# Kernel optimization log

Hardware: AMD Instinct MI355X
Metric: run time of the kernel (lower is better)

The kernel has to match this reference:

```python
import jax, jax.numpy as jnp
import numpy as np

D = 256   # hidden_dim
N = 1024  # total nodes
NP = 384  # paratope nodes
NE = 384  # epitope nodes
NC = 14   # atom channels


def setup_inputs() -> dict:
    key = jax.random.key(0)
    ks = jax.random.split(key, 24)
    s = 1.0 / np.sqrt(D)
    s3 = 1.0 / np.sqrt(3 * D)
    w = lambda k, shape, sc: (jax.random.normal(k, shape, jnp.float32) * sc)
    z = lambda: jnp.zeros((D,), jnp.float32)
    return {
        "H": w(ks[0], (N, D), 1.0),
        "X": w(ks[1], (N, NC, 3), 1.0),
        "paratope_mask": jnp.zeros((N,), bool).at[:NP].set(True),
        "epitope_mask": jnp.zeros((N,), bool).at[NP:NP + NE].set(True),
        "res_w1": w(ks[2], (1, D), 1.0), "res_b1": z(),
        "res_w2": w(ks[3], (D, D), s), "res_b2": z(),
        "atom_w1": w(ks[4], (1, D), 1.0), "atom_b1": z(),
        "atom_w2": w(ks[5], (D, D), s), "atom_b2": z(),
        "sim_weight": jnp.float32(0.5),
        "int_w1": w(ks[6], (3 * D, D), s3), "int_b1": z(),
        "int_w2": w(ks[7], (D, D), s), "int_b2": z(),
        "wl": w(ks[8], (D, D), s),
        "wr": w(ks[9], (D, D), s),
        "wg_w": w(ks[10], (D, D), s), "wg_b": z(),
        "wq_w": w(ks[11], (D, D), s), "wq_b": z(),
        "wk_w": w(ks[12], (D, D), s), "wk_b": z(),
        "wv_w": w(ks[13], (D, D), s), "wv_b": z(),
    }


def _mlp2(x, w1, b1, w2, b2):
    return jax.nn.silu(x @ w1 + b1) @ w2 + b2


def reference(H, X, paratope_mask, epitope_mask,
              res_w1, res_b1, res_w2, res_b2,
              atom_w1, atom_b1, atom_w2, atom_b2,
              sim_weight,
              int_w1, int_b1, int_w2, int_b2,
              wl, wr, wg_w, wg_b, wq_w, wq_b, wk_w, wk_b, wv_w, wv_b):
    p_idx = jnp.nonzero(paratope_mask, size=NP)[0]
    e_idx = jnp.nonzero(epitope_mask, size=NE)[0]
    Hp = H[p_idx]                      # [NP, D]
    He = H[e_idx]                      # [NE, D]
    Xp_ca = X[p_idx, 1]                # [NP, 3] (CA atom)
    Xe_ca = X[e_idx, 1]                # [NE, 3]

    dX = Xp_ca[:, None, :] - Xe_ca[None, :, :]         # [NP, NE, 3]
    S = jnp.sum(dX * dX, axis=-1, keepdims=True)       # [NP, NE, 1]
    # original computes S_residue and S_atom with identical formula
    S_res = _mlp2(S, res_w1, res_b1, res_w2, res_b2)
    S_atom = _mlp2(S, atom_w1, atom_b1, atom_w2, atom_b2)
    wmix = jax.nn.sigmoid(sim_weight)
    S_comb = wmix * S_res + (1.0 - wmix) * S_atom      # [NP, NE, D]

    Hp_e = jnp.broadcast_to(Hp[:, None, :], (NP, NE, D))
    He_e = jnp.broadcast_to(He[None, :, :], (NP, NE, D))
    Z_in = jnp.concatenate([Hp_e, He_e, S_comb], axis=-1)  # [NP, NE, 3D]
    Z = _mlp2(Z_in, int_w1, int_b1, int_w2, int_b2)        # [NP, NE, D]

    I = (Hp @ wl)[:, None, :] * (He @ wr)[None, :, :]      # outer-product interaction
    gate = jax.nn.sigmoid(Z @ wg_w + wg_b)
    f_tri = gate * I

    Q = Z @ wq_w + wq_b
    K = Z @ wk_w + wk_b
    V = Z @ wv_w + wv_b
    scores = jnp.einsum('ped,pfd->pef', Q, K) / (D ** 0.5)  # [NP, NE, NE]
    A = jax.nn.softmax(scores, axis=-1)
    f_att = jnp.einsum('pef,pfd->ped', A, V)

    H_tri = f_tri + f_att                                   # [NP, NE, D]
    return H.at[p_idx].set(H_tri.mean(axis=1))
```

## Files before the change

### kernel.cpp

```cpp
#include <hip/hip_runtime.h>

#define NPAR 384
#define NEPI 384
#define DD   256
#define NTAB 4096
#define SMAX 96.0f
#define SDELTA (SMAX / NTAB)
#define SINVD (NTAB / SMAX)

using bf16x8 = __bf16 __attribute__((ext_vector_type(8)));
using bf16x2 = __bf16 __attribute__((ext_vector_type(2)));
using f32x4  = float __attribute__((ext_vector_type(4)));

#if defined(__has_builtin)
#if __has_builtin(__builtin_amdgcn_cvt_pk_bf16_f32)
#define HAVE_PK_BF16 1
#endif
#endif

__device__ __forceinline__ float sigm(float x) { return 1.0f / (1.0f + __expf(-x)); }
__device__ __forceinline__ float silu(float x) { return x / (1.0f + __expf(-x)); }
__device__ __forceinline__ unsigned short f2bf(float f) {
  unsigned u = __float_as_uint(f);
  u += 0x7fffu + ((u >> 16) & 1u);
  return (unsigned short)(u >> 16);
}
__device__ __forceinline__ float bf2f(unsigned u16) {
  return __uint_as_float(u16 << 16);
}
__device__ __forceinline__ float bf2f_lo(unsigned w) {
  return __uint_as_float(w << 16);
}
__device__ __forceinline__ float bf2f_hi(unsigned w) {
  return __uint_as_float(w & 0xffff0000u);
}
__device__ __forceinline__ uint2 pack4(float a, float b, float c, float d) {
  uint2 r;
#ifdef HAVE_PK_BF16
  bf16x2 lo = __builtin_amdgcn_cvt_pk_bf16_f32(a, b);
  bf16x2 hi = __builtin_amdgcn_cvt_pk_bf16_f32(c, d);
  r.x = __builtin_bit_cast(unsigned, lo);
  r.y = __builtin_bit_cast(unsigned, hi);
#else
  r.x = (unsigned)f2bf(a) | ((unsigned)f2bf(b) << 16);
  r.y = (unsigned)f2bf(c) | ((unsigned)f2bf(d) << 16);
#endif
  return r;
}


__global__ void prep_kernel(
    const float* __restrict__ H, const float* __restrict__ wl,
    const float* __restrict__ wr, const float* __restrict__ int_w1,
    const float* __restrict__ res_w2, const float* __restrict__ atom_w2,
    const float* __restrict__ res_b2, const float* __restrict__ atom_b2,
    const float* __restrict__ int_b1, const float* __restrict__ simw,
    const float* __restrict__ wq_b, const float* __restrict__ wk_w,
    float* __restrict__ Hpl, float* __restrict__ Her,
    float* __restrict__ P1, float* __restrict__ P2,
    float* __restrict__ MrF, float* __restrict__ MaF,
    float* __restrict__ cvec, float* __restrict__ gv,
    float* __restrict__ wkT) {
  __shared__ float tile[32][33];
  const int b = blockIdx.x, t = threadIdx.x;
  if (b < 64) {
    const int bx = b & 7, by = b >> 3;
    const int tx = t & 31, ty = t >> 5;
    for (int r = 0; r < 32; r += 8)
      tile[ty + r][tx] = wk_w[(by * 32 + ty + r) * 256 + bx * 32 + tx];
    __syncthreads();
    for (int r = 0; r < 32; r += 8)
      wkT[(bx * 32 + ty + r) * 256 + by * 32 + tx] = tile[tx][ty + r];
  } else if (b < 576) {
    const int bb = b - 64;
    const int i = bb & 255;
    const bool isMa = bb >= 256;
    const float wmix = 1.0f / (1.0f + __expf(-simw[0]));
    const float sc = isMa ? (1.0f - wmix) : wmix;
    const float* W2 = isMa ? atom_w2 : res_w2;
    float acc = 0.f;
#pragma unroll 8
    for (int k = 0; k < 256; ++k)
      acc += W2[i * 256 + k] * int_w1[(512 + k) * 256 + t];
    (isMa ? MaF : MrF)[i * 256 + t] = acc * sc;
  } else if (b < 584) {
    const int bb = b - 576;
    const float wmix = 1.0f / (1.0f + __expf(-simw[0]));
    float acc = (bb == 0) ? int_b1[t] : 0.f;
#pragma unroll
    for (int k = bb * 32; k < bb * 32 + 32; ++k) {
      float bm = wmix * res_b2[k] + (1.0f - wmix) * atom_b2[k];
      acc += bm * int_w1[(512 + k) * 256 + t];
    }
    atomicAdd(&cvec[t], acc);
  } else if (b < 648) {
    const int lane = t & 63, w = t >> 6;
    const int d = (b - 584) * 4 + w;
    float acc = 0.f;
#pragma unroll
    for (int i = 0; i < 4; ++i) {
      const int c = i * 64 + lane;
      acc += wk_w[d * 256 + c] * wq_b[c];
    }
    acc += __shfl_xor(acc, 1);
    acc += __shfl_xor(acc, 2);
    acc += __shfl_xor(acc, 4);
    acc += __shfl_xor(acc, 8);
    acc += __shfl_xor(acc, 16);
    acc += __shfl_xor(acc, 32);
    if (lane == 0) gv[d] = acc;
  } else {
    const int idx = b - 648;
    const int seg = idx / 384, r = idx % 384;
    const float* A;
    const float* B;
    float* C;
    switch (seg) {
      case 0:  A = H + r * 256;            B = wl;              C = Hpl + r * 256; break;
      case 1:  A = H + (NPAR + r) * 256;   B = wr;              C = Her + r * 256; break;
      case 2:  A = H + r * 256;            B = int_w1;          C = P1 + r * 256;  break;
      default: A = H + (NPAR + r) * 256;   B = int_w1 + 65536;  C = P2 + r * 256;  break;
    }
    float acc = 0.f;
#pragma unroll 8
    for (int k = 0; k < 256; ++k)
      acc += A[k] * B[k * 256 + t];
    C[t] = acc;
  }
}

__global__ void mm_rows(const float* __restrict__ A, const float* __restrict__ B,
                        float* __restrict__ C) {
  const int r = blockIdx.x, j = threadIdx.x;
  float acc = 0.f;
#pragma unroll 8
  for (int k = 0; k < 256; ++k)
    acc += A[r * 256 + k] * B[k * 256 + j];
  C[r * 256 + j] = acc;
}

__global__ void pack_kernel(const float* __restrict__ MrF, const float* __restrict__ MaF,
                            const float* __restrict__ w2, const float* __restrict__ wg,
                            const float* __restrict__ WqkF, unsigned short* __restrict__ wpack) {
  const int idx = blockIdx.x * 256 + threadIdx.x;
  const int m = idx >> 16;
  const int r = idx & 65535;
  const int chunk = r >> 9;
  const int lane = (r >> 3) & 63;
  const int j = r & 7;
  const int k = (chunk >> 4) * 32 + (lane >> 4) * 8 + j;
  const int n = (chunk & 15) * 16 + (lane & 15);
  const float* src;
  switch (m) {
    case 0: src = MrF; break;
    case 1: src = MaF; break;
    case 2: src = w2; break;
    case 3: src = wg; break;
    default: src = WqkF; break;
  }
  wpack[idx] = f2bf(src[k * 256 + n]);
}


__device__ __forceinline__ void zero_acc4(f32x4 (&acc)[4][4]) {
#pragma unroll
  for (int mt = 0; mt < 4; ++mt)
#pragma unroll
    for (int nt = 0; nt < 4; ++nt)
      acc[mt][nt] = (f32x4){0.f, 0.f, 0.f, 0.f};
}

__device__ __forceinline__ void gemm4(f32x4 (&acc)[4][4],
                                      const unsigned short* __restrict__ wp,
                                      const unsigned short* ub, int lane, int wv) {
  const int l15 = lane & 15, l4 = lane >> 4;
#pragma unroll
  for (int ks = 0; ks < 8; ++ks) {
    bf16x8 a[4];
#pragma unroll
    for (int mt = 0; mt < 4; ++mt)
      a[mt] = *reinterpret_cast<const bf16x8*>(wp + ((ks * 16 + wv * 4 + mt) * 64 + lane) * 8);
#pragma unroll
    for (int nt = 0; nt < 4; ++nt) {
      bf16x8 b = *reinterpret_cast<const bf16x8*>(ub + (nt * 16 + l15) * 264 + ks * 32 + l4 * 8);
#pragma unroll
      for (int mt = 0; mt < 4; ++mt)
        acc[mt][nt] = __builtin_amdgcn_mfma_f32_16x16x32_bf16(a[mt], b, acc[mt][nt], 0, 0, 0);
    }
  }
}

__device__ __forceinline__ void fill_u(unsigned short* ub, const float* Sv,
                                       const float* __restrict__ w1,
                                       const float* __restrict__ b1, int t) {
  const int dg = t & 31, rb = t >> 5;
  const f32x4 w1a = *reinterpret_cast<const f32x4*>(&w1[dg * 8]);
  const f32x4 w1b = *reinterpret_cast<const f32x4*>(&w1[dg * 8 + 4]);
  const f32x4 b1a = *reinterpret_cast<const f32x4*>(&b1[dg * 8]);
  const f32x4 b1b = *reinterpret_cast<const f32x4*>(&b1[dg * 8 + 4]);
#pragma unroll
  for (int i = 0; i < 8; ++i) {
    const int e = rb + i * 8;
    const float s = Sv[e];
    uint2 lo = pack4(silu(fmaf(s, w1a[0], b1a[0])), silu(fmaf(s, w1a[1], b1a[1])),
                     silu(fmaf(s, w1a[2], b1a[2])), silu(fmaf(s, w1a[3], b1a[3])));
    uint2 hi = pack4(silu(fmaf(s, w1b[0], b1b[0])), silu(fmaf(s, w1b[1], b1b[1])),
                     silu(fmaf(s, w1b[2], b1b[2])), silu(fmaf(s, w1b[3], b1b[3])));
    uint4 pk = {lo.x, lo.y, hi.x, hi.y};
    *reinterpret_cast<uint4*>(&ub[e * 264 + dg * 8]) = pk;
  }
}


__global__ __launch_bounds__(256, 3) void tab_kernel(
    const float* __restrict__ res_w1, const float* __restrict__ res_b1,
    const float* __restrict__ atom_w1, const float* __restrict__ atom_b1,
    const unsigned short* __restrict__ wpack, unsigned short* __restrict__ tab) {
  __shared__ __align__(16) unsigned short ubuf[64 * 264];
  __shared__ float Sv[64];
  const int t = threadIdx.x, lane = t & 63, wv = t >> 6;
  const int l15 = lane & 15, l4 = lane >> 4;
  const int n0 = blockIdx.x * 64;
  if (t < 64) Sv[t] = (n0 + t) * SDELTA;
  __syncthreads();
  f32x4 acc[4][4];
  zero_acc4(acc);
  fill_u(ubuf, Sv, res_w1, res_b1, t);
  __syncthreads();
  gemm4(acc, wpack + 0 * 65536, ubuf, lane, wv);
  __syncthreads();
  fill_u(ubuf, Sv, atom_w1, atom_b1, t);
  __syncthreads();
  gemm4(acc, wpack + 1 * 65536, ubuf, lane, wv);
#pragma unroll
  for (int mt = 0; mt < 4; ++mt) {
    const int d = wv * 64 + mt * 16 + l4 * 4;
#pragma unroll
    for (int nt = 0; nt < 4; ++nt) {
      const int n = n0 + nt * 16 + l15;
      *reinterpret_cast<uint2*>(&tab[n * 256 + d]) =
          pack4(acc[mt][nt][0], acc[mt][nt][1], acc[mt][nt][2], acc[mt][nt][3]);
    }
  }
}


__global__ __launch_bounds__(256, 3) void pair_kernel(
    const float* __restrict__ Xg, const unsigned short* __restrict__ tab,
    const float* __restrict__ int_b2, const float* __restrict__ wg_b,
    const unsigned short* __restrict__ wpack, const float* __restrict__ cvec,
    const float* __restrict__ P1, const float* __restrict__ P2,
    const float* __restrict__ Hpl, const float* __restrict__ Her,
    float* __restrict__ ftri, unsigned short* __restrict__ Zsw) {
  __shared__ __align__(16) unsigned short ubuf[64 * 264];
  __shared__ float Sv[64];
  __shared__ float pc[DD];
  const int t = threadIdx.x, lane = t & 63, wv = t >> 6;
  const int l15 = lane & 15, l4 = lane >> 4;
  const int p = blockIdx.x / 6, cc = blockIdx.x % 6, e0 = cc * 64;
  const int d0 = wv * 64;

  if (t < 64) {
    const int e = e0 + t;
    float dx = Xg[p * 42 + 3] - Xg[(NPAR + e) * 42 + 3];
    float dy = Xg[p * 42 + 4] - Xg[(NPAR + e) * 42 + 4];
    float dz = Xg[p * 42 + 5] - Xg[(NPAR + e) * 42 + 5];
    Sv[t] = dx * dx + dy * dy + dz * dz;
  }
  pc[t] = P1[p * DD + t] + cvec[t];
  __syncthreads();

  {
    const int dg = t & 31, rb = t >> 5;
    const f32x4 pca = *reinterpret_cast<const f32x4*>(&pc[dg * 8]);
    const f32x4 pcb = *reinterpret_cast<const f32x4*>(&pc[dg * 8 + 4]);
#pragma unroll
    for (int i = 0; i < 8; ++i) {
      const int e = rb + i * 8;
      float sv = Sv[e] * SINVD;
      int idx = (int)sv;
      idx = idx > (NTAB - 2) ? (NTAB - 2) : idx;
      const float fr = sv - (float)idx;
      const uint4 t0 = *reinterpret_cast<const uint4*>(&tab[idx * 256 + dg * 8]);
      const uint4 t1 = *reinterpret_cast<const uint4*>(&tab[(idx + 1) * 256 + dg * 8]);
      const f32x4 p2a = *reinterpret_cast<const f32x4*>(&P2[(e0 + e) * DD + dg * 8]);
      const f32x4 p2b = *reinterpret_cast<const f32x4*>(&P2[(e0 + e) * DD + dg * 8 + 4]);
      float z0 = bf2f_lo(t0.x), z1 = bf2f_hi(t0.x), z2 = bf2f_lo(t0.y), z3 = bf2f_hi(t0.y);
      float z4 = bf2f_lo(t0.z), z5 = bf2f_hi(t0.z), z6 = bf2f_lo(t0.w), z7 = bf2f_hi(t0.w);
      z0 = fmaf(fr, bf2f_lo(t1.x) - z0, z0) + pca[0] + p2a[0];
      z1 = fmaf(fr, bf2f_hi(t1.x) - z1, z1) + pca[1] + p2a[1];
      z2 = fmaf(fr, bf2f_lo(t1.y) - z2, z2) + pca[2] + p2a[2];
      z3 = fmaf(fr, bf2f_hi(t1.y) - z3, z3) + pca[3] + p2a[3];
      z4 = fmaf(fr, bf2f_lo(t1.z) - z4, z4) + pcb[0] + p2b[0];
      z5 = fmaf(fr, bf2f_hi(t1.z) - z5, z5) + pcb[1] + p2b[1];
      z6 = fmaf(fr, bf2f_lo(t1.w) - z6, z6) + pcb[2] + p2b[2];
      z7 = fmaf(fr, bf2f_hi(t1.w) - z7, z7) + pcb[3] + p2b[3];
      uint2 lo = pack4(silu(z0), silu(z1), silu(z2), silu(z3));
      uint2 hi = pack4(silu(z4), silu(z5), silu(z6), silu(z7));
      uint4 pk = {lo.x, lo.y, hi.x, hi.y};
      *reinterpret_cast<uint4*>(&ubuf[e * 264 + dg * 8]) = pk;
    }
  }
  __syncthreads();

  f32x4 acc[4][4];
  zero_acc4(acc);
  gemm4(acc, wpack + 2 * 65536, ubuf, lane, wv);
  __syncthreads();
#pragma unroll
  for (int mt = 0; mt < 4; ++mt) {
    const int d = d0 + mt * 16 + l4 * 4;
    const f32x4 bb = *reinterpret_cast<const f32x4*>(&int_b2[d]);
#pragma unroll
    for (int nt = 0; nt < 4; ++nt) {
      const int e = nt * 16 + l15;
      *reinterpret_cast<uint2*>(&ubuf[e * 264 + d]) =
          pack4(acc[mt][nt][0] + bb[0], acc[mt][nt][1] + bb[1],
                acc[mt][nt][2] + bb[2], acc[mt][nt][3] + bb[3]);
    }
  }
  __syncthreads();

  {
    unsigned short* Zd = Zsw + (size_t)p * 98304 + (size_t)(cc * 4 + wv) * 4096 + lane * 8;
#pragma unroll
    for (int ks = 0; ks < 8; ++ks) {
      *reinterpret_cast<uint4*>(Zd + ks * 512) =
          *reinterpret_cast<const uint4*>(&ubuf[(wv * 16 + l15) * 264 + ks * 32 + l4 * 8]);
    }
  }

  zero_acc4(acc);
  gemm4(acc, wpack + 3 * 65536, ubuf, lane, wv);
#pragma unroll
  for (int mt = 0; mt < 4; ++mt) {
    const int d = d0 + mt * 16 + l4 * 4;
    const f32x4 bb = *reinterpret_cast<const f32x4*>(&wg_b[d]);
    const f32x4 hl = *reinterpret_cast<const f32x4*>(&Hpl[p * DD + d]);
    f32x4 fs = (f32x4){0.f, 0.f, 0.f, 0.f};
#pragma unroll
    for (int nt = 0; nt < 4; ++nt) {
      const int e = e0 + nt * 16 + l15;
      const f32x4 hr = *reinterpret_cast<const f32x4*>(&Her[e * DD + d]);
#pragma unroll
      for (int r = 0; r < 4; ++r)
        fs[r] += sigm(acc[mt][nt][r] + bb[r]) * hr[r];
    }
#pragma unroll
    for (int r = 0; r < 4; ++r) {
      float v = fs[r] * hl[r];
      v += __shfl_xor(v, 1);
      v += __shfl_xor(v, 2);
      v += __shfl_xor(v, 4);
      v += __shfl_xor(v, 8);
      if (l15 == 0) atomicAdd(&ftri[p * DD + d + r], v);
    }
  }
}


__global__ __launch_bounds__(256, 3) void attn_kernel(
    const unsigned short* __restrict__ Zsw, const float* __restrict__ gv,
    const unsigned short* __restrict__ wpack, float* __restrict__ cbufg) {
  __shared__ __align__(16) unsigned short Tc[64 * 264];
  __shared__ float red[256];
  __shared__ float red2[256];
  const int t = threadIdx.x, lane = t & 63, wv = t >> 6;
  const int l15 = lane & 15, l4 = lane >> 4;
  const int xcd = blockIdx.x & 7, inner = blockIdx.x >> 3;
  const int p = (inner / 6) * 8 + xcd, c = inner % 6;
  const unsigned short* Zsp = Zsw + (size_t)p * 98304;
  const unsigned short* wqk = wpack + 4 * 65536;

  {
    f32x4 ta[4][4];
#pragma unroll
    for (int mt = 0; mt < 4; ++mt)
#pragma unroll
      for (int nt = 0; nt < 4; ++nt) ta[mt][nt] = (f32x4){0.f, 0.f, 0.f, 0.f};
    const unsigned short* Tb = Zsp + (size_t)(c * 4) * 4096 + lane * 8;
    bf16x8 bcur[4], bnxt[4];
#pragma unroll
    for (int nt = 0; nt < 4; ++nt)
      bcur[nt] = *reinterpret_cast<const bf16x8*>(Tb + nt * 4096);
#pragma unroll
    for (int ks = 0; ks < 8; ++ks) {
      if (ks < 7) {
#pragma unroll
        for (int nt = 0; nt < 4; ++nt)
          bnxt[nt] = *reinterpret_cast<const bf16x8*>(Tb + nt * 4096 + (ks + 1) * 512);
      }
      bf16x8 a[4];
#pragma unroll
      for (int mt = 0; mt < 4; ++mt)
        a[mt] = *reinterpret_cast<const bf16x8*>(wqk + ((ks * 16 + wv * 4 + mt) * 64 + lane) * 8);
#pragma unroll
      for (int nt = 0; nt < 4; ++nt)
#pragma unroll
        for (int mt = 0; mt < 4; ++mt)
          ta[mt][nt] = __builtin_amdgcn_mfma_f32_16x16x32_bf16(a[mt], bcur[nt], ta[mt][nt], 0, 0, 0);
      if (ks < 7) {
#pragma unroll
        for (int nt = 0; nt < 4; ++nt) bcur[nt] = bnxt[nt];
      }
    }
#pragma unroll
    for (int mt = 0; mt < 4; ++mt) {
      const int d = wv * 64 + mt * 16 + l4 * 4;
      const f32x4 gq = *reinterpret_cast<const f32x4*>(&gv[d]);
#pragma unroll
      for (int nt = 0; nt < 4; ++nt) {
        const int e = nt * 16 + l15;
        *reinterpret_cast<uint2*>(&Tc[e * 264 + d]) =
            pack4((ta[mt][nt][0] + gq[0]) * 0.0625f, (ta[mt][nt][1] + gq[1]) * 0.0625f,
                  (ta[mt][nt][2] + gq[2]) * 0.0625f, (ta[mt][nt][3] + gq[3]) * 0.0625f);
      }
    }
  }
  __syncthreads();

  f32x4 sc[4][6];
#pragma unroll
  for (int mt = 0; mt < 4; ++mt)
#pragma unroll
    for (int s = 0; s < 6; ++s) sc[mt][s] = (f32x4){0.f, 0.f, 0.f, 0.f};

  {
    const unsigned short* Sb = Zsp + (size_t)wv * 4096 + lane * 8;
    bf16x8 b0[3], b1[3];
#pragma unroll
    for (int j = 0; j < 3; ++j)
      b0[j] = *reinterpret_cast<const bf16x8*>(Sb + j * 16384);
#pragma unroll
    for (int ks = 0; ks < 8; ++ks) {
#pragma unroll
      for (int j = 0; j < 3; ++j)
        b1[j] = *reinterpret_cast<const bf16x8*>(Sb + (3 + j) * 16384 + ks * 512);
      bf16x8 a[4];
#pragma unroll
      for (int mt = 0; mt < 4; ++mt)
        a[mt] = *reinterpret_cast<const bf16x8*>(&Tc[(mt * 16 + l15) * 264 + ks * 32 + l4 * 8]);
#pragma unroll
      for (int j = 0; j < 3; ++j)
#pragma unroll
        for (int mt = 0; mt < 4; ++mt)
          sc[mt][j] = __builtin_amdgcn_mfma_f32_16x16x32_bf16(a[mt], b0[j], sc[mt][j], 0, 0, 0);
      if (ks < 7) {
#pragma unroll
        for (int j = 0; j < 3; ++j)
          b0[j] = *reinterpret_cast<const bf16x8*>(Sb + j * 16384 + (ks + 1) * 512);
      }
#pragma unroll
      for (int j = 0; j < 3; ++j)
#pragma unroll
        for (int mt = 0; mt < 4; ++mt)
          sc[mt][3 + j] = __builtin_amdgcn_mfma_f32_16x16x32_bf16(a[mt], b1[j], sc[mt][3 + j], 0, 0, 0);
    }
  }

  float rmax[4][4];
#pragma unroll
  for (int mt = 0; mt < 4; ++mt) {
#pragma unroll
    for (int r = 0; r < 4; ++r) {
      float m = -1e30f;
#pragma unroll
      for (int s = 0; s < 6; ++s) m = fmaxf(m, sc[mt][s][r]);
      m = fmaxf(m, __shfl_xor(m, 1));
      m = fmaxf(m, __shfl_xor(m, 2));
      m = fmaxf(m, __shfl_xor(m, 4));
      m = fmaxf(m, __shfl_xor(m, 8));
      rmax[mt][r] = m;
    }
  }
  if (l15 == 0) {
#pragma unroll
    for (int mt = 0; mt < 4; ++mt)
#pragma unroll
      for (int r = 0; r < 4; ++r)
        red[wv * 64 + mt * 16 + l4 * 4 + r] = rmax[mt][r];
  }
  __syncthreads();
#pragma unroll
  for (int mt = 0; mt < 4; ++mt) {
#pragma unroll
    for (int r = 0; r < 4; ++r) {
      const int row = mt * 16 + l4 * 4 + r;
      rmax[mt][r] = fmaxf(fmaxf(red[row], red[64 + row]), fmaxf(red[128 + row], red[192 + row]));
    }
  }

  float rsum[4][4];
#pragma unroll
  for (int mt = 0; mt < 4; ++mt) {
#pragma unroll
    for (int r = 0; r < 4; ++r) {
      float sSum = 0.f;
#pragma unroll
      for (int s = 0; s < 6; ++s) {
        float e = __expf(sc[mt][s][r] - rmax[mt][r]);
        sc[mt][s][r] = e;
        sSum += e;
      }
      sSum += __shfl_xor(sSum, 1);
      sSum += __shfl_xor(sSum, 2);
      sSum += __shfl_xor(sSum, 4);
      sSum += __shfl_xor(sSum, 8);
      rsum[mt][r] = sSum;
    }
  }
  if (l15 == 0) {
#pragma unroll
    for (int mt = 0; mt < 4; ++mt)
#pragma unroll
      for (int r = 0; r < 4; ++r)
        red2[wv * 64 + mt * 16 + l4 * 4 + r] = rsum[mt][r];
  }
  __syncthreads();
  float rinv[4][4];
#pragma unroll
  for (int mt = 0; mt < 4; ++mt) {
#pragma unroll
    for (int r = 0; r < 4; ++r) {
      const int row = mt * 16 + l4 * 4 + r;
      rinv[mt][r] = 1.0f / (red2[row] + red2[64 + row] + red2[128 + row] + red2[192 + row]);
    }
  }

#pragma unroll
  for (int s = 0; s < 6; ++s) {
    float v = 0.f;
#pragma unroll
    for (int mt = 0; mt < 4; ++mt)
#pragma unroll
      for (int r = 0; r < 4; ++r)
        v += sc[mt][s][r] * rinv[mt][r];
    v += __shfl_xor(v, 16);
    v += __shfl_xor(v, 32);
    if (lane < 16)
      atomicAdd(&cbufg[p * NEPI + s * 64 + wv * 16 + lane], v);
  }
}


__global__ __launch_bounds__(256) void out_kernel(
    const unsigned short* __restrict__ Zsw, const float* __restrict__ ftri,
    const float* __restrict__ cbufg, const float* __restrict__ wvw,
    const float* __restrict__ wvb, float* __restrict__ out) {
  __shared__ float cb[NEPI];
  __shared__ float part[16][257];
  __shared__ float u[DD];
  const int p = blockIdx.x, t = threadIdx.x;
  const int lane = t & 63, wv = t >> 6;
  const int l15 = lane & 15, l4 = lane >> 4;
  for (int i = t; i < NEPI; i += 256) cb[i] = cbufg[p * NEPI + i];
  __syncthreads();
  const unsigned short* Zsp = Zsw + (size_t)p * 98304;
  float a16[16];
#pragma unroll
  for (int j = 0; j < 16; ++j) a16[j] = 0.f;
#pragma unroll 4
  for (int grp = 0; grp < 24; ++grp) {
    const float w = cb[grp * 16 + l15];
    const uint4 z0 = *reinterpret_cast<const uint4*>(Zsp + grp * 4096 + wv * 512 + lane * 8);
    const uint4 z1 = *reinterpret_cast<const uint4*>(Zsp + grp * 4096 + (wv + 4) * 512 + lane * 8);
    a16[0] = fmaf(w, bf2f(z0.x & 0xffffu), a16[0]);
    a16[1] = fmaf(w, bf2f(z0.x >> 16), a16[1]);
    a16[2] = fmaf(w, bf2f(z0.y & 0xffffu), a16[2]);
    a16[3] = fmaf(w, bf2f(z0.y >> 16), a16[3]);
    a16[4] = fmaf(w, bf2f(z0.z & 0xffffu), a16[4]);
    a16[5] = fmaf(w, bf2f(z0.z >> 16), a16[5]);
    a16[6] = fmaf(w, bf2f(z0.w & 0xffffu), a16[6]);
    a16[7] = fmaf(w, bf2f(z0.w >> 16), a16[7]);
    a16[8]  = fmaf(w, bf2f(z1.x & 0xffffu), a16[8]);
    a16[9]  = fmaf(w, bf2f(z1.x >> 16), a16[9]);
    a16[10] = fmaf(w, bf2f(z1.y & 0xffffu), a16[10]);
    a16[11] = fmaf(w, bf2f(z1.y >> 16), a16[11]);
    a16[12] = fmaf(w, bf2f(z1.z & 0xffffu), a16[12]);
    a16[13] = fmaf(w, bf2f(z1.z >> 16), a16[13]);
    a16[14] = fmaf(w, bf2f(z1.w & 0xffffu), a16[14]);
    a16[15] = fmaf(w, bf2f(z1.w >> 16), a16[15]);
  }
#pragma unroll
  for (int j = 0; j < 8; ++j) part[l15][wv * 32 + l4 * 8 + j] = a16[j];
#pragma unroll
  for (int j = 0; j < 8; ++j) part[l15][128 + wv * 32 + l4 * 8 + j] = a16[8 + j];
  __syncthreads();
  float uu = 0.f;
#pragma unroll
  for (int g = 0; g < 16; ++g) uu += part[g][t];
  u[t] = uu;
  __syncthreads();
  float acc = ftri[p * DD + t] + 384.0f * wvb[t];
#pragma unroll 8
  for (int d = 0; d < DD; ++d)
    acc = fmaf(u[d], wvw[d * DD + t], acc);
  out[p * DD + t] = acc * (1.0f / 384.0f);
}


extern "C" void kernel_launch(void* const* d_in, const int* in_sizes, int n_in,
                              void* d_out, int out_size, void* d_ws, size_t ws_size,
                              hipStream_t stream) {
  (void)in_sizes; (void)n_in; (void)out_size; (void)ws_size;
  const float* H = (const float*)d_in[0];
  const float* X = (const float*)d_in[1];
  const float* res_w1 = (const float*)d_in[4];
  const float* res_b1 = (const float*)d_in[5];
  const float* res_w2 = (const float*)d_in[6];
  const float* res_b2 = (const float*)d_in[7];
  const float* atom_w1 = (const float*)d_in[8];
  const float* atom_b1 = (const float*)d_in[9];
  const float* atom_w2 = (const float*)d_in[10];
  const float* atom_b2 = (const float*)d_in[11];
  const float* simw = (const float*)d_in[12];
  const float* int_w1 = (const float*)d_in[13];
  const float* int_b1 = (const float*)d_in[14];
  const float* int_w2 = (const float*)d_in[15];
  const float* int_b2 = (const float*)d_in[16];
  const float* wl = (const float*)d_in[17];
  const float* wr = (const float*)d_in[18];
  const float* wg_w = (const float*)d_in[19];
  const float* wg_b = (const float*)d_in[20];
  const float* wq_w = (const float*)d_in[21];
  const float* wq_b = (const float*)d_in[22];
  const float* wk_w = (const float*)d_in[23];
  const float* wv_w = (const float*)d_in[25];
  const float* wv_b = (const float*)d_in[26];

  char* ws = (char*)d_ws;
  unsigned short* wpack = (unsigned short*)(ws + 0);
  float* MrF   = (float*)(ws + 655360);
  float* MaF   = (float*)(ws + 917504);
  float* WqkF  = (float*)(ws + 1179648);
  float* wkT   = (float*)(ws + 1441792);
  float* cvec  = (float*)(ws + 1703936);
  float* gv    = (float*)(ws + 1704960);
  float* P1    = (float*)(ws + 1705984);
  float* P2    = (float*)(ws + 2099200);
  float* Hpl   = (float*)(ws + 2492416);
  float* Her   = (float*)(ws + 2885632);
  float* ftri  = (float*)(ws + 3278848);
  float* cbufg = (float*)(ws + 3672064);
  unsigned short* Zsw = (unsigned short*)(ws + 4261888);
  unsigned short* tab = (unsigned short*)(ws + 79759360);

  hipMemsetAsync(ftri, 0, 393216 + 589824, stream);
  hipMemsetAsync(cvec, 0, DD * sizeof(float), stream);
  prep_kernel<<<2184, 256, 0, stream>>>(H, wl, wr, int_w1, res_w2, atom_w2,
                                        res_b2, atom_b2, int_b1, simw, wq_b, wk_w,
                                        Hpl, Her, P1, P2, MrF, MaF, cvec, gv, wkT);
  mm_rows<<<256, 256, 0, stream>>>(wq_w, wkT, WqkF);
  pack_kernel<<<1280, 256, 0, stream>>>(MrF, MaF, int_w2, wg_w, WqkF, wpack);
  tab_kernel<<<NTAB / 64, 256, 0, stream>>>(res_w1, res_b1, atom_w1, atom_b1, wpack, tab);
  pair_kernel<<<2304, 256, 0, stream>>>(X, tab, int_b2, wg_b, wpack, cvec,
                                        P1, P2, Hpl, Her, ftri, Zsw);
  attn_kernel<<<2304, 256, 0, stream>>>(Zsw, gv, wpack, cbufg);
  out_kernel<<<384, 256, 0, stream>>>(Zsw, ftri, cbufg, wv_w, wv_b, (float*)d_out);
  hipMemcpyAsync((float*)d_out + NPAR * DD, H + NPAR * DD,
                 (1024 - NPAR) * DD * sizeof(float), hipMemcpyDeviceToDevice, stream);
}
```

Baseline: 347.4 us.

## Drop Wq·Wk precompute, apply Wq and Wk as two GEMMs, fuse out-stage into attention

Removes the fp32 Wq·Wk^T product kernel (mm_rows) and the wk transpose. Attention now multiplies Z by Wq, stages the result in LDS, then multiplies by packed Wk^T, which adds a second bf16 GEMM per block. The attention kernel also computes the softmax-weighted Z sum itself, using the Z tile it already has, and atomically adds into a per-p buffer. This leaves a small out2 kernel that only does the final Wv matvec. The aim is fewer launches and less serial prep work, at the cost of more MFMA work and an extra bf16 rounding in the attention path.

```diff
diff --git a/kernel.cpp b/kernel.cpp
--- a/kernel.cpp
+++ b/kernel.cpp
@@ -59,22 +59,11 @@
     float* __restrict__ Hpl, float* __restrict__ Her,
     float* __restrict__ P1, float* __restrict__ P2,
     float* __restrict__ MrF, float* __restrict__ MaF,
-    float* __restrict__ cvec, float* __restrict__ gv,
-    float* __restrict__ wkT) {
-  __shared__ float tile[32][33];
+    float* __restrict__ cvec, float* __restrict__ gv) {
   const int b = blockIdx.x, t = threadIdx.x;
-  if (b < 64) {
-    const int bx = b & 7, by = b >> 3;
-    const int tx = t & 31, ty = t >> 5;
-    for (int r = 0; r < 32; r += 8)
-      tile[ty + r][tx] = wk_w[(by * 32 + ty + r) * 256 + bx * 32 + tx];
-    __syncthreads();
-    for (int r = 0; r < 32; r += 8)
-      wkT[(bx * 32 + ty + r) * 256 + by * 32 + tx] = tile[tx][ty + r];
-  } else if (b < 576) {
-    const int bb = b - 64;
-    const int i = bb & 255;
-    const bool isMa = bb >= 256;
+  if (b < 512) {
+    const int i = b & 255;
+    const bool isMa = b >= 256;
     const float wmix = 1.0f / (1.0f + __expf(-simw[0]));
     const float sc = isMa ? (1.0f - wmix) : wmix;
     const float* W2 = isMa ? atom_w2 : res_w2;
@@ -83,8 +72,8 @@
     for (int k = 0; k < 256; ++k)
       acc += W2[i * 256 + k] * int_w1[(512 + k) * 256 + t];
     (isMa ? MaF : MrF)[i * 256 + t] = acc * sc;
-  } else if (b < 584) {
-    const int bb = b - 576;
+  } else if (b < 520) {
+    const int bb = b - 512;
     const float wmix = 1.0f / (1.0f + __expf(-simw[0]));
     float acc = (bb == 0) ? int_b1[t] : 0.f;
 #pragma unroll
@@ -93,9 +82,9 @@
       acc += bm * int_w1[(512 + k) * 256 + t];
     }
     atomicAdd(&cvec[t], acc);
-  } else if (b < 648) {
+  } else if (b < 584) {
     const int lane = t & 63, w = t >> 6;
-    const int d = (b - 584) * 4 + w;
+    const int d = (b - 520) * 4 + w;
     float acc = 0.f;
 #pragma unroll
     for (int i = 0; i < 4; ++i) {
@@ -110,7 +99,7 @@
     acc += __shfl_xor(acc, 32);
     if (lane == 0) gv[d] = acc;
   } else {
-    const int idx = b - 648;
+    const int idx = b - 584;
     const int seg = idx / 384, r = idx % 384;
     const float* A;
     const float* B;
@@ -129,19 +118,10 @@
   }
 }
 
-__global__ void mm_rows(const float* __restrict__ A, const float* __restrict__ B,
-                        float* __restrict__ C) {
-  const int r = blockIdx.x, j = threadIdx.x;
-  float acc = 0.f;
-#pragma unroll 8
-  for (int k = 0; k < 256; ++k)
-    acc += A[r * 256 + k] * B[k * 256 + j];
-  C[r * 256 + j] = acc;
-}
-
 __global__ void pack_kernel(const float* __restrict__ MrF, const float* __restrict__ MaF,
                             const float* __restrict__ w2, const float* __restrict__ wg,
-                            const float* __restrict__ WqkF, unsigned short* __restrict__ wpack) {
+                            const float* __restrict__ wq, const float* __restrict__ wk,
+                            unsigned short* __restrict__ wpack) {
   const int idx = blockIdx.x * 256 + threadIdx.x;
   const int m = idx >> 16;
   const int r = idx & 65535;
@@ -151,14 +131,16 @@
   const int k = (chunk >> 4) * 32 + (lane >> 4) * 8 + j;
   const int n = (chunk & 15) * 16 + (lane & 15);
   const float* src;
+  bool swap = false;
   switch (m) {
     case 0: src = MrF; break;
     case 1: src = MaF; break;
     case 2: src = w2; break;
     case 3: src = wg; break;
-    default: src = WqkF; break;
-  }
-  wpack[idx] = f2bf(src[k * 256 + n]);
+    case 4: src = wq; break;
+    default: src = wk; swap = true; break;
+  }
+  wpack[idx] = f2bf(swap ? src[n * 256 + k] : src[k * 256 + n]);
 }
 
 
@@ -361,7 +343,7 @@
 
 __global__ __launch_bounds__(256, 3) void attn_kernel(
     const unsigned short* __restrict__ Zsw, const float* __restrict__ gv,
-    const unsigned short* __restrict__ wpack, float* __restrict__ cbufg) {
+    const unsigned short* __restrict__ wpack, float* __restrict__ ubufg) {
   __shared__ __align__(16) unsigned short Tc[64 * 264];
   __shared__ float red[256];
   __shared__ float red2[256];
@@ -370,14 +352,12 @@
   const int xcd = blockIdx.x & 7, inner = blockIdx.x >> 3;
   const int p = (inner / 6) * 8 + xcd, c = inner % 6;
   const unsigned short* Zsp = Zsw + (size_t)p * 98304;
-  const unsigned short* wqk = wpack + 4 * 65536;
+  const unsigned short* wq_p = wpack + 4 * 65536;
+  const unsigned short* wkT_p = wpack + 5 * 65536;
 
   {
     f32x4 ta[4][4];
-#pragma unroll
-    for (int mt = 0; mt < 4; ++mt)
-#pragma unroll
-      for (int nt = 0; nt < 4; ++nt) ta[mt][nt] = (f32x4){0.f, 0.f, 0.f, 0.f};
+    zero_acc4(ta);
     const unsigned short* Tb = Zsp + (size_t)(c * 4) * 4096 + lane * 8;
     bf16x8 bcur[4], bnxt[4];
 #pragma unroll
@@ -393,7 +373,7 @@
       bf16x8 a[4];
 #pragma unroll
       for (int mt = 0; mt < 4; ++mt)
-        a[mt] = *reinterpret_cast<const bf16x8*>(wqk + ((ks * 16 + wv * 4 + mt) * 64 + lane) * 8);
+        a[mt] = *reinterpret_cast<const bf16x8*>(wq_p + ((ks * 16 + wv * 4 + mt) * 64 + lane) * 8);
 #pragma unroll
       for (int nt = 0; nt < 4; ++nt)
 #pragma unroll
@@ -404,6 +384,24 @@
         for (int nt = 0; nt < 4; ++nt) bcur[nt] = bnxt[nt];
       }
     }
+#pragma unroll
+    for (int mt = 0; mt < 4; ++mt) {
+      const int d = wv * 64 + mt * 16 + l4 * 4;
+#pragma unroll
+      for (int nt = 0; nt < 4; ++nt) {
+        const int e = nt * 16 + l15;
+        *reinterpret_cast<uint2*>(&Tc[e * 264 + d]) =
+            pack4(ta[mt][nt][0], ta[mt][nt][1], ta[mt][nt][2], ta[mt][nt][3]);
+      }
+    }
+  }
+  __syncthreads();
+
+  {
+    f32x4 ta[4][4];
+    zero_acc4(ta);
+    gemm4(ta, wkT_p, Tc, lane, wv);
+    __syncthreads();
 #pragma unroll
     for (int mt = 0; mt < 4; ++mt) {
       const int d = wv * 64 + mt * 16 + l4 * 4;
@@ -424,7 +422,6 @@
   for (int mt = 0; mt < 4; ++mt)
 #pragma unroll
     for (int s = 0; s < 6; ++s) sc[mt][s] = (f32x4){0.f, 0.f, 0.f, 0.f};
-
   {
     const unsigned short* Sb = Zsp + (size_t)wv * 4096 + lane * 8;
     bf16x8 b0[3], b1[3];
@@ -527,6 +524,8 @@
     }
   }
 
+  float* cpart = reinterpret_cast<float*>(&Tc[0]);
+  float* part = reinterpret_cast<float*>(&Tc[1024]);
 #pragma unroll
   for (int s = 0; s < 6; ++s) {
     float v = 0.f;
@@ -537,31 +536,16 @@
         v += sc[mt][s][r] * rinv[mt][r];
     v += __shfl_xor(v, 16);
     v += __shfl_xor(v, 32);
-    if (lane < 16)
-      atomicAdd(&cbufg[p * NEPI + s * 64 + wv * 16 + lane], v);
-  }
-}
-
-
-__global__ __launch_bounds__(256) void out_kernel(
-    const unsigned short* __restrict__ Zsw, const float* __restrict__ ftri,
-    const float* __restrict__ cbufg, const float* __restrict__ wvw,
-    const float* __restrict__ wvb, float* __restrict__ out) {
-  __shared__ float cb[NEPI];
-  __shared__ float part[16][257];
-  __shared__ float u[DD];
-  const int p = blockIdx.x, t = threadIdx.x;
-  const int lane = t & 63, wv = t >> 6;
-  const int l15 = lane & 15, l4 = lane >> 4;
-  for (int i = t; i < NEPI; i += 256) cb[i] = cbufg[p * NEPI + i];
-  __syncthreads();
-  const unsigned short* Zsp = Zsw + (size_t)p * 98304;
+    if (lane < 16) cpart[s * 64 + wv * 16 + lane] = v;
+  }
+  __syncthreads();
+
   float a16[16];
 #pragma unroll
   for (int j = 0; j < 16; ++j) a16[j] = 0.f;
 #pragma unroll 4
   for (int grp = 0; grp < 24; ++grp) {
-    const float w = cb[grp * 16 + l15];
+    const float w = cpart[grp * 16 + l15];
     const uint4 z0 = *reinterpret_cast<const uint4*>(Zsp + grp * 4096 + wv * 512 + lane * 8);
     const uint4 z1 = *reinterpret_cast<const uint4*>(Zsp + grp * 4096 + (wv + 4) * 512 + lane * 8);
     a16[0] = fmaf(w, bf2f(z0.x & 0xffffu), a16[0]);
@@ -582,14 +566,24 @@
     a16[15] = fmaf(w, bf2f(z1.w >> 16), a16[15]);
   }
 #pragma unroll
-  for (int j = 0; j < 8; ++j) part[l15][wv * 32 + l4 * 8 + j] = a16[j];
-#pragma unroll
-  for (int j = 0; j < 8; ++j) part[l15][128 + wv * 32 + l4 * 8 + j] = a16[8 + j];
+  for (int j = 0; j < 8; ++j) part[l15 * 257 + wv * 32 + l4 * 8 + j] = a16[j];
+#pragma unroll
+  for (int j = 0; j < 8; ++j) part[l15 * 257 + 128 + wv * 32 + l4 * 8 + j] = a16[8 + j];
   __syncthreads();
   float uu = 0.f;
 #pragma unroll
-  for (int g = 0; g < 16; ++g) uu += part[g][t];
-  u[t] = uu;
+  for (int g = 0; g < 16; ++g) uu += part[g * 257 + t];
+  atomicAdd(&ubufg[p * DD + t], uu);
+}
+
+
+__global__ __launch_bounds__(256) void out2_kernel(
+    const float* __restrict__ ubufg, const float* __restrict__ ftri,
+    const float* __restrict__ wvw, const float* __restrict__ wvb,
+    float* __restrict__ out) {
+  __shared__ float u[DD];
+  const int p = blockIdx.x, t = threadIdx.x;
+  u[t] = ubufg[p * DD + t];
   __syncthreads();
   float acc = ftri[p * DD + t] + 384.0f * wvb[t];
 #pragma unroll 8
@@ -630,33 +624,30 @@
 
   char* ws = (char*)d_ws;
   unsigned short* wpack = (unsigned short*)(ws + 0);
-  float* MrF   = (float*)(ws + 655360);
-  float* MaF   = (float*)(ws + 917504);
-  float* WqkF  = (float*)(ws + 1179648);
-  float* wkT   = (float*)(ws + 1441792);
-  float* cvec  = (float*)(ws + 1703936);
-  float* gv    = (float*)(ws + 1704960);
-  float* P1    = (float*)(ws + 1705984);
-  float* P2    = (float*)(ws + 2099200);
-  float* Hpl   = (float*)(ws + 2492416);
-  float* Her   = (float*)(ws + 2885632);
-  float* ftri  = (float*)(ws + 3278848);
-  float* cbufg = (float*)(ws + 3672064);
-  unsigned short* Zsw = (unsigned short*)(ws + 4261888);
-  unsigned short* tab = (unsigned short*)(ws + 79759360);
-
-  hipMemsetAsync(ftri, 0, 393216 + 589824, stream);
+  float* MrF   = (float*)(ws + 786432);
+  float* MaF   = (float*)(ws + 1048576);
+  float* cvec  = (float*)(ws + 1310720);
+  float* gv    = (float*)(ws + 1311744);
+  float* P1    = (float*)(ws + 1312768);
+  float* P2    = (float*)(ws + 1705984);
+  float* Hpl   = (float*)(ws + 2099200);
+  float* Her   = (float*)(ws + 2492416);
+  float* ftri  = (float*)(ws + 2885632);
+  float* ubufg = (float*)(ws + 3278848);
+  unsigned short* Zsw = (unsigned short*)(ws + 3672064);
+  unsigned short* tab = (unsigned short*)(ws + 79169536);
+
+  hipMemsetAsync(ftri, 0, 393216 + 393216, stream);
   hipMemsetAsync(cvec, 0, DD * sizeof(float), stream);
-  prep_kernel<<<2184, 256, 0, stream>>>(H, wl, wr, int_w1, res_w2, atom_w2,
+  prep_kernel<<<2120, 256, 0, stream>>>(H, wl, wr, int_w1, res_w2, atom_w2,
                                         res_b2, atom_b2, int_b1, simw, wq_b, wk_w,
-                                        Hpl, Her, P1, P2, MrF, MaF, cvec, gv, wkT);
-  mm_rows<<<256, 256, 0, stream>>>(wq_w, wkT, WqkF);
-  pack_kernel<<<1280, 256, 0, stream>>>(MrF, MaF, int_w2, wg_w, WqkF, wpack);
+                                        Hpl, Her, P1, P2, MrF, MaF, cvec, gv);
+  pack_kernel<<<1536, 256, 0, stream>>>(MrF, MaF, int_w2, wg_w, wq_w, wk_w, wpack);
   tab_kernel<<<NTAB / 64, 256, 0, stream>>>(res_w1, res_b1, atom_w1, atom_b1, wpack, tab);
   pair_kernel<<<2304, 256, 0, stream>>>(X, tab, int_b2, wg_b, wpack, cvec,
                                         P1, P2, Hpl, Her, ftri, Zsw);
-  attn_kernel<<<2304, 256, 0, stream>>>(Zsw, gv, wpack, cbufg);
-  out_kernel<<<384, 256, 0, stream>>>(Zsw, ftri, cbufg, wv_w, wv_b, (float*)d_out);
+  attn_kernel<<<2304, 256, 0, stream>>>(Zsw, gv, wpack, ubufg);
+  out2_kernel<<<384, 256, 0, stream>>>(ubufg, ftri, wv_w, wv_b, (float*)d_out);
   hipMemcpyAsync((float*)d_out + NPAR * DD, H + NPAR * DD,
                  (1024 - NPAR) * DD * sizeof(float), hipMemcpyDeviceToDevice, stream);
 }
```

Result: slower. 366.1 us (+5.4%).
